# Optimization experiments

Measured on AMD Instinct MI355X. Metric: run time of the kernel, lower is better.

Reference implementation:

```python
import jax, jax.numpy as jnp
import numpy as np

NUM_GRAPHS = 128

def _gcn_conv(x, W, b, src, dst, deg_inv_sqrt, n_nodes):
    # PyG GCNConv: h = X W; out[dst] += d^-1/2[src] * d^-1/2[dst] * h[src]; out += b
    h = x @ W
    norm = deg_inv_sqrt[src] * deg_inv_sqrt[dst]  # [E]
    msg = h[src] * norm[:, None]                  # [E, C]
    out = jax.ops.segment_sum(msg, dst, num_segments=n_nodes)
    return out + b


def setup_inputs() -> dict:
    key = jax.random.key(0)
    k1, k2, k3, k4, k5 = jax.random.split(key, 5)
    n_nodes, n_edges, c_in, c_hid = 50000, 800000, 256, 256
    x = jax.random.normal(k1, (n_nodes, c_in), dtype=jnp.float32)
    edge_index = jax.random.randint(k2, (2, n_edges), 0, n_nodes, dtype=jnp.int64)
    batch = jnp.sort(jax.random.randint(k3, (n_nodes,), 0, NUM_GRAPHS, dtype=jnp.int64))
    s1 = 1.0 / np.sqrt(c_in)
    s2 = 1.0 / np.sqrt(c_hid)
    W1 = jax.random.uniform(k4, (c_in, c_hid), jnp.float32, -s1, s1)
    b1 = jnp.zeros((c_hid,), jnp.float32)
    W2 = jax.random.uniform(k5, (c_hid, c_hid), jnp.float32, -s2, s2)
    b2 = jnp.zeros((c_hid,), jnp.float32)
    return {"x": x, "edge_index": edge_index, "batch": batch,
            "W1": W1, "b1": b1, "W2": W2, "b2": b2}


def reference(x, edge_index, batch, W1, b1, W2, b2):
    n_nodes = x.shape[0]
    # add self-loops (GCNConv default add_self_loops=True)
    loops = jnp.arange(n_nodes, dtype=edge_index.dtype)
    src = jnp.concatenate([edge_index[0], loops])
    dst = jnp.concatenate([edge_index[1], loops])
    deg = jax.ops.segment_sum(jnp.ones_like(dst, dtype=x.dtype), dst, num_segments=n_nodes)
    deg_inv_sqrt = jnp.where(deg > 0, jax.lax.rsqrt(deg), 0.0)

    h = jax.nn.relu(_gcn_conv(x, W1, b1, src, dst, deg_inv_sqrt, n_nodes))
    # dropout p=0.2 is identity in eval mode
    h = jax.nn.relu(_gcn_conv(h, W2, b2, src, dst, deg_inv_sqrt, n_nodes))

    # global mean pool over graph ids
    sums = jax.ops.segment_sum(h, batch, num_segments=NUM_GRAPHS)
    cnts = jax.ops.segment_sum(jnp.ones((n_nodes,), h.dtype), batch, num_segments=NUM_GRAPHS)
    return sums / jnp.maximum(cnts, 1.0)[:, None]
```

## Files before the change

### kernel.cpp

```cpp
#include <hip/hip_runtime.h>

#define NCH 256
#define NS  16

typedef short short8 __attribute__((ext_vector_type(8)));
typedef float f32x4  __attribute__((ext_vector_type(4)));

__device__ __forceinline__ float b2f(unsigned short u) {
    union { unsigned int i; float f; } x; x.i = ((unsigned int)u) << 16; return x.f;
}
__device__ __forceinline__ unsigned short f2b(float f) {
    unsigned int u = __float_as_uint(f);
    unsigned int r = (u + 0x7FFFu + ((u >> 16) & 1u)) >> 16;
    return (unsigned short)r;
}

#define GLOAD_LDS16(gptr, lptr) \
    __builtin_amdgcn_global_load_lds((const __attribute__((address_space(1))) void*)(gptr), \
                                     (__attribute__((address_space(3))) void*)(lptr), 16, 0, 0)

__global__ __launch_bounds__(256) void k_pre(const int* __restrict__ dst, int E,
                                             int* __restrict__ deg, int nh,
                                             unsigned shmul,
                                             const float* __restrict__ W1,
                                             const float* __restrict__ W2,
                                             unsigned short* __restrict__ Wt1,
                                             unsigned short* __restrict__ Wt2) {
    int b = blockIdx.x;
    if (b < nh) {
        const int shard  = b & 7;
        const int nchunk = nh >> 3;
        const int chunk  = b >> 3;
        const int per = (E + nchunk - 1) / nchunk;
        const int e0 = chunk * per;
        const int e1 = min(e0 + per, E);
        for (int e = e0 + threadIdx.x; e < e1; e += 256) {
            int d = dst[e];
            if ((int)__umulhi((unsigned)d, shmul) == shard)
                atomicAdd(&deg[d], 1);
        }
    } else {
        int k = (b - nh) & 255;
        const float* W = ((b - nh) >> 8) ? W2 : W1;
        unsigned short* Wt = ((b - nh) >> 8) ? Wt2 : Wt1;
        int n = threadIdx.x;
        Wt[(size_t)n * 256 + k] = f2b(W[(size_t)k * 256 + n]);
    }
}

__global__ __launch_bounds__(256) void k_scan_blk(const int* __restrict__ deg,
                                                  int* __restrict__ part,
                                                  int* __restrict__ bsum, int N) {
    __shared__ int sm[256];
    int t = threadIdx.x;
    int base = blockIdx.x * 1024 + t * 4;
    int v[4]; int s = 0;
#pragma unroll
    for (int j = 0; j < 4; ++j) {
        int i = base + j;
        int d = (i < N) ? deg[i] : 0;
        v[j] = d; s += d;
    }
    sm[t] = s; __syncthreads();
#pragma unroll
    for (int off = 1; off < 256; off <<= 1) {
        int u = (t >= off) ? sm[t - off] : 0;
        __syncthreads();
        sm[t] += u;
        __syncthreads();
    }
    int excl = sm[t] - s;
#pragma unroll
    for (int j = 0; j < 4; ++j) {
        int i = base + j;
        if (i < N) part[i] = excl;
        excl += v[j];
    }
    if (t == 255) bsum[blockIdx.x] = sm[255];
}

__global__ void k_scan_top(int* __restrict__ bsum, int nb, int* __restrict__ rowptr_end) {
    int t = threadIdx.x;
    int orig = (t < nb) ? bsum[t] : 0;
    int v = orig;
#pragma unroll
    for (int off = 1; off < 64; off <<= 1) {
        int u = __shfl_up(v, off, 64);
        if (t >= off) v += u;
    }
    if (t < nb) bsum[t] = v - orig;
    if (t == 63) *rowptr_end = v;
}

__global__ __launch_bounds__(256) void k_finalize(const int* __restrict__ deg,
                                                  int* __restrict__ row_ptr,
                                                  const int* __restrict__ boff,
                                                  int* __restrict__ cursor,
                                                  float* __restrict__ dinv, int N) {
    int i = blockIdx.x * 256 + threadIdx.x;
    if (i < N) {
        int rp = row_ptr[i] + boff[i >> 10];
        row_ptr[i] = rp;
        cursor[i]  = rp;
        dinv[i] = rsqrtf((float)(deg[i] + 1));
    }
}

__device__ __forceinline__ void load_bfr(const unsigned short* __restrict__ Bt,
                                         short8 bfr[2][8], int w, int lr, int ku) {
    const unsigned short* pb = Bt + (size_t)(w * 32 + lr) * NCH + ku * 8;
#pragma unroll
    for (int nf = 0; nf < 2; ++nf)
#pragma unroll
        for (int ks = 0; ks < 8; ++ks)
            bfr[nf][ks] = *(const short8*)(pb + nf * 16 * NCH + ks * 32);
}

__device__ __forceinline__ void gemm_compute_store(const unsigned short* As,
                                                   const short8 bfr[2][8],
                                                   unsigned short* __restrict__ C,
                                                   int M, int t, int w, int lr, int ku) {
    f32x4 acc[2][2];
#pragma unroll
    for (int rf = 0; rf < 2; ++rf)
#pragma unroll
        for (int nf = 0; nf < 2; ++nf) acc[rf][nf] = (f32x4){0.f, 0.f, 0.f, 0.f};

#pragma unroll
    for (int ks = 0; ks < 8; ++ks) {
#pragma unroll
        for (int rf = 0; rf < 2; ++rf) {
            int row = rf * 16 + lr;
            int uu  = (ks * 4 + ku) ^ (row & 7);
            short8 af = *(const short8*)&As[row * 256 + uu * 8];
            acc[rf][0] = __builtin_amdgcn_mfma_f32_16x16x32_bf16(bfr[0][ks], af,
                                                                 acc[rf][0], 0, 0, 0);
            acc[rf][1] = __builtin_amdgcn_mfma_f32_16x16x32_bf16(bfr[1][ks], af,
                                                                 acc[rf][1], 0, 0, 0);
        }
    }

#pragma unroll
    for (int rf = 0; rf < 2; ++rf) {
        int row = t * 32 + rf * 16 + lr;
        if (row < M) {
            unsigned short* pc = C + (size_t)row * NCH + w * 32 + ku * 4;
#pragma unroll
            for (int nf = 0; nf < 2; ++nf) {
                unsigned short us[4];
                us[0] = f2b(acc[rf][nf][0]); us[1] = f2b(acc[rf][nf][1]);
                us[2] = f2b(acc[rf][nf][2]); us[3] = f2b(acc[rf][nf][3]);
                *(int2*)(pc + nf * 16) = *(const int2*)us;
            }
        }
    }
}

__global__ __launch_bounds__(512, 4) void k_gemm2(const unsigned short* __restrict__ A,
                                                  const unsigned short* __restrict__ Bt,
                                                  unsigned short* __restrict__ C,
                                                  int M, int tiles) {
    __shared__ unsigned short As[2][32 * 256];
    const int tid  = threadIdx.x;
    const int w    = tid >> 6;
    const int lane = tid & 63;
    const int lr   = lane & 15;
    const int ku   = lane >> 4;

    short8 bfr[2][8];
    load_bfr(Bt, bfr, w, lr, ku);

    const int gu0 = w * 128 + lane;

#define STAGE2(tt, buf) do {                                                  \
        _Pragma("unroll")                                                     \
        for (int j = 0; j < 2; ++j) {                                         \
            int gu = gu0 + j * 64;                                            \
            int r  = gu >> 5;                                                 \
            int u  = gu & 31;                                                 \
            int grow = (tt) * 32 + r; if (grow >= M) grow = M - 1;            \
            const unsigned short* gp = A + (size_t)grow * NCH +               \
                                       ((u ^ (r & 7)) << 3);                  \
            GLOAD_LDS16(gp, (buf) + (size_t)(w * 128 + j * 64) * 8);          \
        }                                                                     \
    } while (0)

    int t = blockIdx.x;
    int cur = 0;
    if (t < tiles) STAGE2(t, As[0]);
    __syncthreads();

    for (; t < tiles; t += gridDim.x) {
        int tn = t + gridDim.x;
        if (tn < tiles) STAGE2(tn, As[cur ^ 1]);
        gemm_compute_store(As[cur], bfr, C, M, t, w, lr, ku);
        __syncthreads();
        cur ^= 1;
    }
#undef STAGE2
}

__global__ __launch_bounds__(512, 4) void k_gemm1s(const float* __restrict__ A,
                                                   const unsigned short* __restrict__ Bt,
                                                   unsigned short* __restrict__ C,
                                                   int M, int tiles, int gblocks,
                                                   const int* __restrict__ src,
                                                   const int* __restrict__ dst, int E,
                                                   int* __restrict__ cursor,
                                                   const float* __restrict__ dinv,
                                                   int2* __restrict__ cw,
                                                   unsigned shmul) {
    __shared__ unsigned short As[2][32 * 256];
    const int tid = threadIdx.x;

    if (blockIdx.x >= gblocks) {
        const int b = blockIdx.x - gblocks;
        const int shard  = b & 7;
        const int nchunk = (gridDim.x - gblocks) >> 3;
        const int chunk  = b >> 3;
        const int per = (E + nchunk - 1) / nchunk;
        const int e0 = chunk * per;
        const int e1 = min(e0 + per, E);
        for (int e = e0 + tid; e < e1; e += 512) {
            int d = dst[e];
            int s = (int)__umulhi((unsigned)d, shmul);
            if (s == shard) {
                int sv = src[e];
                int pos = atomicAdd(&cursor[d], 1);
                cw[pos] = make_int2(sv, __float_as_int(dinv[sv]));
            }
        }
        return;
    }

    const int w    = tid >> 6;
    const int lane = tid & 63;
    const int lr   = lane & 15;
    const int ku   = lane >> 4;

    short8 bfr[2][8];
    load_bfr(Bt, bfr, w, lr, ku);

    const int r0_ = tid >> 5,          u0_ = tid & 31;
    const int r1_ = (tid + 512) >> 5,  u1_ = (tid + 512) & 31;

    int t = blockIdx.x;
    int cur = 0;
    if (t < tiles) {
        int g0 = t * 32 + r0_; if (g0 >= M) g0 = M - 1;
        int g1 = t * 32 + r1_; if (g1 >= M) g1 = M - 1;
        const float4* pa0 = (const float4*)(A + (size_t)g0 * NCH + u0_ * 8);
        const float4* pa1 = (const float4*)(A + (size_t)g1 * NCH + u1_ * 8);
        float4 a0 = pa0[0], a1 = pa0[1];
        float4 b0 = pa1[0], b1 = pa1[1];
        unsigned short us[8];
        us[0]=f2b(a0.x); us[1]=f2b(a0.y); us[2]=f2b(a0.z); us[3]=f2b(a0.w);
        us[4]=f2b(a1.x); us[5]=f2b(a1.y); us[6]=f2b(a1.z); us[7]=f2b(a1.w);
        *(int4*)&As[0][r0_ * 256 + ((u0_ ^ (r0_ & 7)) << 3)] = *(const int4*)us;
        us[0]=f2b(b0.x); us[1]=f2b(b0.y); us[2]=f2b(b0.z); us[3]=f2b(b0.w);
        us[4]=f2b(b1.x); us[5]=f2b(b1.y); us[6]=f2b(b1.z); us[7]=f2b(b1.w);
        *(int4*)&As[0][r1_ * 256 + ((u1_ ^ (r1_ & 7)) << 3)] = *(const int4*)us;
    }
    __syncthreads();

    for (; t < tiles; t += gblocks) {
        int tn = t + gblocks;
        float4 a0, a1, b0, b1;
        if (tn < tiles) {
            int g0 = tn * 32 + r0_; if (g0 >= M) g0 = M - 1;
            int g1 = tn * 32 + r1_; if (g1 >= M) g1 = M - 1;
            const float4* pa0 = (const float4*)(A + (size_t)g0 * NCH + u0_ * 8);
            const float4* pa1 = (const float4*)(A + (size_t)g1 * NCH + u1_ * 8);
            a0 = pa0[0]; a1 = pa0[1];
            b0 = pa1[0]; b1 = pa1[1];
        }

        gemm_compute_store(As[cur], bfr, C, M, t, w, lr, ku);

        if (tn < tiles) {
            unsigned short us[8];
            us[0]=f2b(a0.x); us[1]=f2b(a0.y); us[2]=f2b(a0.z); us[3]=f2b(a0.w);
            us[4]=f2b(a1.x); us[5]=f2b(a1.y); us[6]=f2b(a1.z); us[7]=f2b(a1.w);
            *(int4*)&As[cur ^ 1][r0_ * 256 + ((u0_ ^ (r0_ & 7)) << 3)] = *(const int4*)us;
            us[0]=f2b(b0.x); us[1]=f2b(b0.y); us[2]=f2b(b0.z); us[3]=f2b(b0.w);
            us[4]=f2b(b1.x); us[5]=f2b(b1.y); us[6]=f2b(b1.z); us[7]=f2b(b1.w);
            *(int4*)&As[cur ^ 1][r1_ * 256 + ((u1_ ^ (r1_ & 7)) << 3)] = *(const int4*)us;
        }
        __syncthreads();
        cur ^= 1;
    }
}

__global__ __launch_bounds__(256) void k_agg_w(const unsigned short* __restrict__ h,
                                               const float* __restrict__ dinv,
                                               const int* __restrict__ row_ptr,
                                               const int2* __restrict__ cw,
                                               const float* __restrict__ bias,
                                               unsigned short* __restrict__ out, int M) {
    int v = blockIdx.x * 4 + (threadIdx.x >> 6);
    if (v >= M) return;
    const int lane = threadIdx.x & 63;
    const int half = lane >> 5;
    const int cb   = (lane & 31) << 3;

    float acc[8] = {};
    float dv = dinv[v];

    short8 rs = {};
    if (half == 0) rs = *(const short8*)&h[(size_t)v * NCH + cb];

    int beg = row_ptr[v], end = row_ptr[v + 1];
    int i0 = beg + half * 2;

    short8 r0 = {}, r1 = {};
    float  w0 = 0.f, w1 = 0.f;
    bool b0 = i0 < end, b1 = i0 + 1 < end;
    if (b0) {
        int2 e = cw[i0];
        r0 = *(const short8*)&h[(size_t)e.x * NCH + cb];
        w0 = __int_as_float(e.y);
    }
    if (b1) {
        int2 e = cw[i0 + 1];
        r1 = *(const short8*)&h[(size_t)e.x * NCH + cb];
        w1 = __int_as_float(e.y);
    }

    while (b0) {
        int in = i0 + 4;
        bool n0 = in < end, n1 = in + 1 < end;
        short8 s0 = {}, s1 = {};
        float  x0 = 0.f, x1 = 0.f;
        if (n0) {
            int2 e = cw[in];
            s0 = *(const short8*)&h[(size_t)e.x * NCH + cb];
            x0 = __int_as_float(e.y);
        }
        if (n1) {
            int2 e = cw[in + 1];
            s1 = *(const short8*)&h[(size_t)e.x * NCH + cb];
            x1 = __int_as_float(e.y);
        }
#pragma unroll
        for (int i = 0; i < 8; ++i) acc[i] += w0 * b2f((unsigned short)r0[i]);
#pragma unroll
        for (int i = 0; i < 8; ++i) acc[i] += w1 * b2f((unsigned short)r1[i]);
        r0 = s0; r1 = s1; w0 = x0; w1 = x1; b0 = n0; b1 = n1; i0 = in;
    }

    if (half == 0) {
#pragma unroll
        for (int i = 0; i < 8; ++i) acc[i] += dv * b2f((unsigned short)rs[i]);
    }

#pragma unroll
    for (int i = 0; i < 8; ++i) acc[i] += __shfl_xor(acc[i], 32, 64);

    if (half == 0) {
        f32x4 bl = *(const f32x4*)&bias[cb];
        f32x4 bh = *(const f32x4*)&bias[cb + 4];
        unsigned short us[8];
#pragma unroll
        for (int i = 0; i < 8; ++i) {
            float b = (i < 4) ? bl[i] : bh[i - 4];
            us[i] = f2b(fmaxf(dv * acc[i] + b, 0.0f));
        }
        *(int4*)&out[(size_t)v * NCH + cb] = *(const int4*)us;
    }
}

__device__ __forceinline__ int lower_bound_i(const int* a, int n, int key) {
    int lo = 0, hi = n;
    while (lo < hi) {
        int mid = (lo + hi) >> 1;
        if (a[mid] < key) lo = mid + 1; else hi = mid;
    }
    return lo;
}

__global__ __launch_bounds__(64) void k_pool_a(const unsigned short* __restrict__ a,
                                               const int* __restrict__ batch,
                                               float* __restrict__ partial, int N) {
    int g = blockIdx.x, s = blockIdx.y;
    const int lane = threadIdx.x;
    const int half = lane >> 5;
    const int cb   = (lane & 31) << 3;

    int lo = lower_bound_i(batch, N, g);
    int hi = lower_bound_i(batch, N, g + 1);
    int cnt = hi - lo;
    int len = (cnt + NS - 1) / NS;
    int rlo = lo + s * len;
    int rhi = min(rlo + len, hi);

    float acc[8] = {};
    for (int r = rlo + half; r < rhi; r += 2) {
        short8 hv = *(const short8*)&a[(size_t)r * NCH + cb];
#pragma unroll
        for (int i = 0; i < 8; ++i) acc[i] += b2f((unsigned short)hv[i]);
    }
#pragma unroll
    for (int i = 0; i < 8; ++i) acc[i] += __shfl_xor(acc[i], 32, 64);

    if (half == 0) {
        float* p = partial + ((size_t)g * NS + s) * NCH + cb;
        *(f32x4*)p       = (f32x4){acc[0], acc[1], acc[2], acc[3]};
        *(f32x4*)(p + 4) = (f32x4){acc[4], acc[5], acc[6], acc[7]};
    }
}

__global__ __launch_bounds__(256) void k_pool_b(const float* __restrict__ partial,
                                                const int* __restrict__ batch,
                                                float* __restrict__ out, int N) {
    int g = blockIdx.x, ch = threadIdx.x;
    int lo = lower_bound_i(batch, N, g);
    int hi = lower_bound_i(batch, N, g + 1);
    float s = 0.0f;
#pragma unroll
    for (int k = 0; k < NS; ++k)
        s += partial[((size_t)g * NS + k) * NCH + ch];
    out[(size_t)g * NCH + ch] = s / (float)max(hi - lo, 1);
}

extern "C" void kernel_launch(void* const* d_in, const int* in_sizes, int n_in,
                              void* d_out, int out_size, void* d_ws, size_t ws_size,
                              hipStream_t stream) {
    const float* x     = (const float*)d_in[0];
    const int*   ei    = (const int*)d_in[1];
    const int*   batch = (const int*)d_in[2];
    const float* W1    = (const float*)d_in[3];
    const float* b1    = (const float*)d_in[4];
    const float* W2    = (const float*)d_in[5];
    const float* b2    = (const float*)d_in[6];
    float* out = (float*)d_out;

    const int M = in_sizes[0] / NCH;
    const int E = in_sizes[1] / 2;
    const int* src = ei;
    const int* dst = ei + E;

    char* w = (char*)d_ws;
    auto alloc = [&](size_t bytes) -> void* {
        void* p = (void*)w;
        w += (bytes + 255) & ~(size_t)255;
        return p;
    };
    int*   deg     = (int*)alloc((size_t)M * 4);
    float* dinv    = (float*)alloc((size_t)M * 4);
    int*   row_ptr = (int*)alloc((size_t)(M + 1) * 4);
    int*   cursor  = (int*)alloc((size_t)M * 4);
    int*   bsum    = (int*)alloc(64 * 4);
    int2*  cw      = (int2*)alloc((size_t)E * 8);
    unsigned short* bufP = (unsigned short*)alloc((size_t)M * NCH * 2);
    unsigned short* bufQ = (unsigned short*)alloc((size_t)M * NCH * 2);
    unsigned short* Wt1  = (unsigned short*)alloc((size_t)NCH * NCH * 2);
    unsigned short* Wt2  = (unsigned short*)alloc((size_t)NCH * NCH * 2);
    float* partial = (float*)alloc((size_t)128 * NS * NCH * 4);

    const int nb = (M + 1023) / 1024;
    const unsigned shmul = (unsigned)(((8ull << 32) + M - 1) / (unsigned long long)M);
    const int tiles = (M + 31) / 32;
    const int nh = 2048;
    const int gblocks = 512;
    const int sblocks = 2048;

    (void)hipMemsetAsync(deg, 0, (size_t)M * 4, stream);
    k_pre<<<nh + 512, 256, 0, stream>>>(dst, E, deg, nh, shmul, W1, W2, Wt1, Wt2);
    k_scan_blk<<<nb, 256, 0, stream>>>(deg, row_ptr, bsum, M);
    k_scan_top<<<1, 64, 0, stream>>>(bsum, nb, row_ptr + M);
    k_finalize<<<(M + 255) / 256, 256, 0, stream>>>(deg, row_ptr, bsum, cursor, dinv, M);

    const int agrid = (M + 3) / 4;

    k_gemm1s<<<gblocks + sblocks, 512, 0, stream>>>(x, Wt1, bufP, M, tiles, gblocks,
                                                    src, dst, E, cursor, dinv, cw, shmul);
    k_agg_w<<<agrid, 256, 0, stream>>>(bufP, dinv, row_ptr, cw, b1, bufQ, M);
    k_gemm2<<<512, 512, 0, stream>>>(bufQ, Wt2, bufP, M, tiles);
    k_agg_w<<<agrid, 256, 0, stream>>>(bufP, dinv, row_ptr, cw, b2, bufQ, M);
    k_pool_a<<<dim3(128, NS), 64, 0, stream>>>(bufQ, batch, partial, M);
    k_pool_b<<<128, 256, 0, stream>>>(partial, batch, out, M);
}
```

Measured before the change: 272.4 us.

## Overlap degree histogram with GEMM1 and move CSR scatter to its own kernel

The degree-counting atomics now run in extra blocks of the first GEMM kernel instead of a separate pre-kernel. The CSR edge scatter, which was previously co-scheduled with GEMM1, becomes a standalone kernel launched after the scan and finalize steps. Weight transpose-casting gets its own small kernel. The intent is to hide the histogram pass behind GEMM1, but the scatter pass is now exposed and serialized, and there is one more launch.

```diff
diff --git a/kernel.cpp b/kernel.cpp
--- a/kernel.cpp
+++ b/kernel.cpp
@@ -19,33 +19,14 @@
     __builtin_amdgcn_global_load_lds((const __attribute__((address_space(1))) void*)(gptr), \
                                      (__attribute__((address_space(3))) void*)(lptr), 16, 0, 0)
 
-__global__ __launch_bounds__(256) void k_pre(const int* __restrict__ dst, int E,
-                                             int* __restrict__ deg, int nh,
-                                             unsigned shmul,
-                                             const float* __restrict__ W1,
-                                             const float* __restrict__ W2,
-                                             unsigned short* __restrict__ Wt1,
-                                             unsigned short* __restrict__ Wt2) {
-    int b = blockIdx.x;
-    if (b < nh) {
-        const int shard  = b & 7;
-        const int nchunk = nh >> 3;
-        const int chunk  = b >> 3;
-        const int per = (E + nchunk - 1) / nchunk;
-        const int e0 = chunk * per;
-        const int e1 = min(e0 + per, E);
-        for (int e = e0 + threadIdx.x; e < e1; e += 256) {
-            int d = dst[e];
-            if ((int)__umulhi((unsigned)d, shmul) == shard)
-                atomicAdd(&deg[d], 1);
-        }
-    } else {
-        int k = (b - nh) & 255;
-        const float* W = ((b - nh) >> 8) ? W2 : W1;
-        unsigned short* Wt = ((b - nh) >> 8) ? Wt2 : Wt1;
-        int n = threadIdx.x;
-        Wt[(size_t)n * 256 + k] = f2b(W[(size_t)k * 256 + n]);
-    }
+__global__ __launch_bounds__(256) void k_castT(const float* __restrict__ W1,
+                                               const float* __restrict__ W2,
+                                               unsigned short* __restrict__ Wt1,
+                                               unsigned short* __restrict__ Wt2) {
+    int k = blockIdx.x, n = threadIdx.x;
+    const float* W = blockIdx.y ? W2 : W1;
+    unsigned short* Wt = blockIdx.y ? Wt2 : Wt1;
+    Wt[(size_t)n * 256 + k] = f2b(W[(size_t)k * 256 + n]);
 }
 
 __global__ __launch_bounds__(256) void k_scan_blk(const int* __restrict__ deg,
@@ -103,6 +84,29 @@
         row_ptr[i] = rp;
         cursor[i]  = rp;
         dinv[i] = rsqrtf((float)(deg[i] + 1));
+    }
+}
+
+__global__ __launch_bounds__(256) void k_scatter_sh(const int* __restrict__ src,
+                                                    const int* __restrict__ dst, int E,
+                                                    int* __restrict__ cursor,
+                                                    const float* __restrict__ dinv,
+                                                    int2* __restrict__ cw,
+                                                    unsigned shmul) {
+    const int shard  = blockIdx.x & 7;
+    const int nchunk = gridDim.x >> 3;
+    const int chunk  = blockIdx.x >> 3;
+    const int per = (E + nchunk - 1) / nchunk;
+    const int e0 = chunk * per;
+    const int e1 = min(e0 + per, E);
+    for (int e = e0 + threadIdx.x; e < e1; e += 256) {
+        int d = dst[e];
+        int s = (int)__umulhi((unsigned)d, shmul);
+        if (s == shard) {
+            int sv = src[e];
+            int pos = atomicAdd(&cursor[d], 1);
+            cw[pos] = make_int2(sv, __float_as_int(dinv[sv]));
+        }
     }
 }
 
@@ -200,16 +204,13 @@
 #undef STAGE2
 }
 
-__global__ __launch_bounds__(512, 4) void k_gemm1s(const float* __restrict__ A,
-                                                   const unsigned short* __restrict__ Bt,
-                                                   unsigned short* __restrict__ C,
-                                                   int M, int tiles, int gblocks,
-                                                   const int* __restrict__ src,
-                                                   const int* __restrict__ dst, int E,
-                                                   int* __restrict__ cursor,
-                                                   const float* __restrict__ dinv,
-                                                   int2* __restrict__ cw,
-                                                   unsigned shmul) {
+__global__ __launch_bounds__(512, 4) void k_g1h(const float* __restrict__ A,
+                                                const unsigned short* __restrict__ Bt,
+                                                unsigned short* __restrict__ C,
+                                                int M, int tiles, int gblocks,
+                                                const int* __restrict__ dst, int E,
+                                                int* __restrict__ deg,
+                                                unsigned shmul) {
     __shared__ unsigned short As[2][32 * 256];
     const int tid = threadIdx.x;
 
@@ -223,12 +224,8 @@
         const int e1 = min(e0 + per, E);
         for (int e = e0 + tid; e < e1; e += 512) {
             int d = dst[e];
-            int s = (int)__umulhi((unsigned)d, shmul);
-            if (s == shard) {
-                int sv = src[e];
-                int pos = atomicAdd(&cursor[d], 1);
-                cw[pos] = make_int2(sv, __float_as_int(dinv[sv]));
-            }
+            if ((int)__umulhi((unsigned)d, shmul) == shard)
+                atomicAdd(&deg[d], 1);
         }
         return;
     }
@@ -460,20 +457,21 @@
     const int nb = (M + 1023) / 1024;
     const unsigned shmul = (unsigned)(((8ull << 32) + M - 1) / (unsigned long long)M);
     const int tiles = (M + 31) / 32;
-    const int nh = 2048;
     const int gblocks = 512;
-    const int sblocks = 2048;
+    const int hblocks = 2048;
 
     (void)hipMemsetAsync(deg, 0, (size_t)M * 4, stream);
-    k_pre<<<nh + 512, 256, 0, stream>>>(dst, E, deg, nh, shmul, W1, W2, Wt1, Wt2);
+    k_castT<<<dim3(256, 2), 256, 0, stream>>>(W1, W2, Wt1, Wt2);
+
+    k_g1h<<<gblocks + hblocks, 512, 0, stream>>>(x, Wt1, bufP, M, tiles, gblocks,
+                                                 dst, E, deg, shmul);
     k_scan_blk<<<nb, 256, 0, stream>>>(deg, row_ptr, bsum, M);
     k_scan_top<<<1, 64, 0, stream>>>(bsum, nb, row_ptr + M);
     k_finalize<<<(M + 255) / 256, 256, 0, stream>>>(deg, row_ptr, bsum, cursor, dinv, M);
+    k_scatter_sh<<<2048, 256, 0, stream>>>(src, dst, E, cursor, dinv, cw, shmul);
 
     const int agrid = (M + 3) / 4;
 
-    k_gemm1s<<<gblocks + sblocks, 512, 0, stream>>>(x, Wt1, bufP, M, tiles, gblocks,
-                                                    src, dst, E, cursor, dinv, cw, shmul);
     k_agg_w<<<agrid, 256, 0, stream>>>(bufP, dinv, row_ptr, cw, b1, bufQ, M);
     k_gemm2<<<512, 512, 0, stream>>>(bufQ, Wt2, bufP, M, tiles);
     k_agg_w<<<agrid, 256, 0, stream>>>(bufP, dinv, row_ptr, cw, b2, bufQ, M);
```

Result: no change. 272.7 us (+0.1%).
